# Optimization experiments

Hardware: AMD Instinct MI355X
Metric: run time of the kernel (lower is better)

## Reference

```python
import jax, jax.numpy as jnp
import numpy as np

H = 256
NUM_REL = 480
NUM_ENT = 23000
N_TRIPLES = 8192
T = 10  # cur_ts == path_len window


def _lin_params(key, din, dout):
    kw, _ = jax.random.split(key)
    W = jax.random.normal(kw, (din, dout), dtype=jnp.float32) * 0.02
    b = jnp.zeros((dout,), dtype=jnp.float32)
    return W, b


def setup_inputs() -> dict:
    key = jax.random.key(0)
    ks = jax.random.split(key, 16)
    pre_emb = jax.random.normal(ks[0], (NUM_ENT, H), dtype=jnp.float32)
    r_emb = jax.random.normal(ks[1], (NUM_REL, H), dtype=jnp.float32)
    # history counts: sparse non-negative (zeros are masked to -1e9 in softmax)
    part = jax.random.uniform(ks[2], (N_TRIPLES, T * NUM_REL), dtype=jnp.float32)
    mask = jax.random.uniform(ks[3], (N_TRIPLES, T * NUM_REL)) < 0.3
    partial_embeding = jnp.where(mask, part, 0.0)
    sub_idx = jax.random.randint(ks[4], (N_TRIPLES,), 0, NUM_ENT)
    rel_idx = jax.random.randint(ks[5], (N_TRIPLES,), 0, NUM_REL)
    obj_idx = jax.random.randint(ks[6], (N_TRIPLES,), 0, NUM_ENT)
    Wm1, bm1 = _lin_params(ks[7], H, 2 * H)
    Wm2, bm2 = _lin_params(ks[8], 2 * H, H)
    Wattn, battn = _lin_params(ks[9], H, H)
    Wh1, bh1 = _lin_params(ks[10], H, H)
    Wh2, bh2 = _lin_params(ks[11], H, H)
    Walign, balign = _lin_params(ks[12], H, H)
    Wih = jax.random.normal(ks[13], (H, 3 * H), dtype=jnp.float32) * 0.02
    Whh = jax.random.normal(ks[14], (H, 3 * H), dtype=jnp.float32) * 0.02
    bih = jnp.zeros((3 * H,), dtype=jnp.float32)
    bhh = jnp.zeros((3 * H,), dtype=jnp.float32)
    return dict(pre_emb=pre_emb, r_emb=r_emb, partial_embeding=partial_embeding,
                sub_idx=sub_idx, rel_idx=rel_idx, obj_idx=obj_idx, cur_ts=T,
                Wm1=Wm1, bm1=bm1, Wm2=Wm2, bm2=bm2, Wattn=Wattn, battn=battn,
                Wh1=Wh1, bh1=bh1, Wh2=Wh2, bh2=bh2, Walign=Walign, balign=balign,
                Wih=Wih, Whh=Whh, bih=bih, bhh=bhh)


def _gru_cell(x, h, Wih, Whh, bih, bhh):
    # torch.nn.GRUCell math
    gi = x @ Wih + bih
    gh = h @ Whh + bhh
    i_r, i_z, i_n = jnp.split(gi, 3, axis=-1)
    h_r, h_z, h_n = jnp.split(gh, 3, axis=-1)
    r = jax.nn.sigmoid(i_r + h_r)
    z = jax.nn.sigmoid(i_z + h_z)
    n = jnp.tanh(i_n + r * h_n)
    return (1.0 - z) * n + z * h


def reference(pre_emb, r_emb, partial_embeding, sub_idx, rel_idx, obj_idx, cur_ts,
              Wm1, bm1, Wm2, bm2, Wattn, battn, Wh1, bh1, Wh2, bh2,
              Walign, balign, Wih, Whh, bih, bhh):
    n = partial_embeding.shape[0]
    num_rel = r_emb.shape[0]
    t = cur_ts  # path window covers [0, cur_ts)
    # relation mapping
    mapped_rel = (r_emb @ Wm1 + bm1) @ Wm2 + bm2            # [R, H]
    q_rel = mapped_rel[rel_idx]                               # [N, H]
    # attention logits base (loop-invariant): q W_attn mapped_rel^T
    base = (q_rel @ Wattn + battn) @ mapped_rel.T            # [N, R]
    # [N, t*R] -> [t, N, R] time-major slices
    hist = partial_embeding[:, : t * num_rel].reshape(n, t, num_rel).swapaxes(0, 1)
    h0 = jnp.zeros((n, mapped_rel.shape[1]), dtype=pre_emb.dtype)

    def step(h, cur):
        attn = cur * base
        attn = jax.nn.softmax(jnp.where(attn == 0, -1e9, attn), axis=1)
        x = attn @ mapped_rel                                 # [N, H]
        return _gru_cell(x, h, Wih, Whh, bih, bhh), None

    gru_hidden, _ = jax.lax.scan(step, h0, hist)
    # predicted history + match loss
    predicted_hist = 0.1 * ((q_rel @ Wh1 + bh1) @ Wh2 + bh2) + q_rel
    match_loss = jnp.mean((predicted_hist - gru_hidden) ** 2)
    # forward_forth (distmult)
    h2 = _gru_cell(q_rel, predicted_hist, Wih, Whh, bih, bhh)  # [N, H]
    sub = pre_emb[sub_idx]
    score_ = ((sub @ Walign + balign) * h2) @ (pre_emb @ Walign + balign).T  # [N, E]
    # BCE(sigmoid(score_), one_hot(obj)): per-elem -y*logsig(s) - (1-y)*logsig(-s)
    pos = score_[jnp.arange(n), obj_idx]
    path_loss = (-jnp.sum(jax.nn.log_sigmoid(-score_)) - jnp.sum(pos)) / (score_.size)
    score = jax.nn.sigmoid(score_)
    return match_loss, path_loss, score
```

## Files before the change

### kernel.cpp

```cpp
#include <hip/hip_runtime.h>
#include <hip/hip_bf16.h>
#include <stdint.h>

#define DEV __device__ __forceinline__

typedef unsigned short u16;
typedef __attribute__((ext_vector_type(8))) short bf16x8;
typedef __attribute__((ext_vector_type(4))) float f32x4;
typedef __attribute__((ext_vector_type(4))) unsigned short u16x4;

constexpr int H  = 256;
constexpr int R  = 480;
constexpr int RP = 512;
constexpr int NE = 23000;
constexpr int NT = 8192;
constexpr int TT = 10;

DEV u16 f2b(float f) {
  union { float f; unsigned u; } x; x.f = f;
  unsigned u = x.u;
  return (u16)((u + 0x7fffu + ((u >> 16) & 1u)) >> 16);
}
DEV float b2f(u16 h) {
  union { unsigned u; float f; } x; x.u = ((unsigned)h) << 16;
  return x.f;
}

DEV void gload_lds16(const u16* g, u16* lds) {
  __builtin_amdgcn_global_load_lds(
      (const __attribute__((address_space(1))) unsigned int*)g,
      (__attribute__((address_space(3))) unsigned int*)lds, 16, 0, 0);
}

__launch_bounds__(256)
__global__ void stageA_k(const float* __restrict__ r_emb,
                         const float* __restrict__ Wm1, const float* __restrict__ bm1,
                         const float* __restrict__ Wm2, const float* __restrict__ bm2,
                         const float* __restrict__ Wattn, const float* __restrict__ battn,
                         const float* __restrict__ Wih,
                         const float* __restrict__ Wh1, const float* __restrict__ bh1,
                         const float* __restrict__ Wh2, const float* __restrict__ bh2,
                         const float* __restrict__ Whh, const float* __restrict__ bhh,
                         const float* __restrict__ bih, const float* __restrict__ Walign,
                         float* __restrict__ mapped, float* __restrict__ t1,
                         float* __restrict__ Pg, float* __restrict__ G2,
                         u16* __restrict__ MWT, u16* __restrict__ WhhT,
                         u16* __restrict__ WalignT, float* __restrict__ bsum) {
  __shared__ float re[256], hid[512], mp[256], p1l[256], Pl[256];
  const int j = threadIdx.x;
  if (blockIdx.x >= 480) {
    const int b = blockIdx.x - 480;
    if (b < 768) {
      WhhT[(size_t)b * 256 + j] = f2b(Whh[(size_t)j * 768 + b]);
    } else if (b < 1024) {
      const int n = b - 768;
      WalignT[(size_t)n * 256 + j] = f2b(Walign[(size_t)j * 256 + n]);
    } else {
      const int c = (b - 1024) * 256 + j;
      if (c < 768) bsum[c] = bih[c] + (c < 512 ? bhh[c] : 0.f);
    }
    return;
  }
  const int r = blockIdx.x;
  re[j] = r_emb[(size_t)r * 256 + j];
  __syncthreads();
  float s0 = bm1[j], s1 = bm1[j + 256];
  for (int k = 0; k < 256; ++k) {
    const float a = re[k];
    s0 += a * Wm1[(size_t)k * 512 + j];
    s1 += a * Wm1[(size_t)k * 512 + j + 256];
  }
  hid[j] = s0; hid[j + 256] = s1;
  __syncthreads();
  float m = bm2[j];
  for (int k = 0; k < 512; ++k) m += hid[k] * Wm2[(size_t)k * 256 + j];
  mp[j] = m; mapped[(size_t)r * 256 + j] = m;
  __syncthreads();
  float tv = battn[j];
  for (int k = 0; k < 256; ++k) tv += mp[k] * Wattn[(size_t)k * 256 + j];
  t1[(size_t)r * 256 + j] = tv;
  float mw0 = 0.f, mw1 = 0.f, mw2 = 0.f;
  for (int k = 0; k < 256; ++k) {
    const float a = mp[k];
    mw0 += a * Wih[(size_t)k * 768 + j];
    mw1 += a * Wih[(size_t)k * 768 + j + 256];
    mw2 += a * Wih[(size_t)k * 768 + j + 512];
  }
  MWT[(size_t)j * RP + r] = f2b(mw0);
  MWT[(size_t)(j + 256) * RP + r] = f2b(mw1);
  MWT[(size_t)(j + 512) * RP + r] = f2b(mw2);
  float pv = bh1[j];
  for (int k = 0; k < 256; ++k) pv += mp[k] * Wh1[(size_t)k * 256 + j];
  p1l[j] = pv;
  __syncthreads();
  float Pv = bh2[j];
  for (int k = 0; k < 256; ++k) Pv += p1l[k] * Wh2[(size_t)k * 256 + j];
  Pv = 0.1f * Pv + mp[j];
  Pl[j] = Pv; Pg[(size_t)r * 256 + j] = Pv;
  __syncthreads();
  float pw0 = bhh[j], pw1 = bhh[j + 256], pw2 = bhh[j + 512];
  for (int k = 0; k < 256; ++k) {
    const float a = Pl[k];
    pw0 += a * Whh[(size_t)k * 768 + j];
    pw1 += a * Whh[(size_t)k * 768 + j + 256];
    pw2 += a * Whh[(size_t)k * 768 + j + 512];
  }
  const float rg = 1.f / (1.f + __expf(-(mw0 + bih[j] + pw0)));
  const float zg = 1.f / (1.f + __expf(-(mw1 + bih[j + 256] + pw1)));
  const float ng = tanhf(mw2 + bih[j + 512] + rg * pw2);
  G2[(size_t)r * 256 + j] = (1.f - zg) * ng + zg * Pv;
}

__global__ void sgemm_bt_k(const float* __restrict__ A, const float* __restrict__ W,
                           float* __restrict__ C, int M, int N, int K) {
  const int idx = blockIdx.x * 256 + threadIdx.x;
  if (idx >= M * N) return;
  const int i = idx / N, j = idx % N;
  float s = 0.f;
  const float* a = A + (size_t)i * K;
  const float* w = W + (size_t)j * K;
  for (int k = 0; k < K; ++k) s += a[k] * w[k];
  C[idx] = s;
}

__global__ void softmax_all_k(const float* __restrict__ part, const float* __restrict__ B480,
                              const int* __restrict__ rel_idx, u16* __restrict__ attn) {
  const int task = blockIdx.x * 4 + (threadIdx.x >> 6);
  const int lane = threadIdx.x & 63;
  const int tt = task >> 13;
  const int i  = task & (NT - 1);
  const float* cur = part + (size_t)i * (TT * R) + (size_t)tt * R;
  const float* b = B480 + (size_t)rel_idx[i] * R;
  float v[8];
  float m = -3e38f;
  #pragma unroll
  for (int j = 0; j < 8; ++j) {
    const int r = lane + j * 64;
    float val = -1e9f;
    if (r < R) {
      const float c = cur[r];
      val = (c == 0.f) ? -1e9f : c * b[r];
      m = fmaxf(m, val);
    }
    v[j] = val;
  }
  #pragma unroll
  for (int o = 32; o; o >>= 1) m = fmaxf(m, __shfl_xor(m, o));
  float s = 0.f;
  #pragma unroll
  for (int j = 0; j < 8; ++j) {
    const int r = lane + j * 64;
    if (r < R) { v[j] = __expf(v[j] - m); s += v[j]; }
  }
  #pragma unroll
  for (int o = 32; o; o >>= 1) s += __shfl_xor(s, o);
  const float inv = 1.f / s;
  u16* arow = attn + (size_t)task * RP;
  #pragma unroll
  for (int j = 0; j < 8; ++j) {
    const int r = lane + j * 64;
    arow[r] = (r < R) ? f2b(v[j] * inv) : (u16)0;
  }
}

__launch_bounds__(256)
__global__ void scan_k(const u16* __restrict__ WhhT, const float* __restrict__ bhh,
                       const u16* __restrict__ gi_all, float* __restrict__ hbuf) {
  __shared__ __align__(16) u16 As[32 * 256];
  __shared__ __align__(16) u16 Bs[2][192 * 64];
  const int tid = threadIdx.x;
  const int lane = tid & 63;
  const int wv = tid >> 6;
  const int rf = wv >> 1;
  const int ch = wv & 1;
  const int fr = lane & 15;
  const int fq = lane >> 4;
  const int row_l = rf * 16 + fr;
  const int grow = blockIdx.x * 32 + row_l;
  const int sw = (fr & 7) * 8;

  auto stageB = [&](int buf, int cg, int k0) {
    #pragma unroll
    for (int it = 0; it < 6; ++it) {
      const int c = it * 256 + tid;
      const int vr = c >> 3, s = c & 7;
      const int vcol = ((vr >> 6) * 256) + cg * 64 + (vr & 63);
      gload_lds16(WhhT + (size_t)vcol * 256 + k0 + ((s ^ (vr & 7)) * 8),
                  &Bs[buf][(it * 256 + wv * 64) * 8]);
    }
  };

  float hreg[4][2][4];
  #pragma unroll
  for (int cg = 0; cg < 4; ++cg)
    #pragma unroll
    for (int nn = 0; nn < 2; ++nn)
      #pragma unroll
      for (int j = 0; j < 4; ++j) hreg[cg][nn][j] = 0.f;

  for (int t = 0; t < TT; ++t) {
    const u16* gi = gi_all + (size_t)t * NT * 768;
    #pragma unroll
    for (int cg = 0; cg < 4; ++cg) {
      f32x4 acc[6] = {};
      u16x4 gv[3][2];
      #pragma unroll
      for (int nn = 0; nn < 2; ++nn) {
        const int c = cg * 64 + ch * 32 + nn * 16 + fq * 4;
        const size_t gb = (size_t)grow * 768 + c;
        gv[0][nn] = *(const u16x4*)&gi[gb];
        gv[1][nn] = *(const u16x4*)&gi[gb + 256];
        gv[2][nn] = *(const u16x4*)&gi[gb + 512];
      }
      if (t > 0) {
        stageB(0, cg, 0);
        #pragma unroll
        for (int ki = 0; ki < 4; ++ki) {
          const int cb = ki & 1;
          if (ki < 3) {
            stageB(cb ^ 1, cg, (ki + 1) * 64);
            asm volatile("s_waitcnt vmcnt(6)" ::: "memory");
          } else {
            asm volatile("s_waitcnt vmcnt(0)" ::: "memory");
          }
          __builtin_amdgcn_sched_barrier(0);
          __builtin_amdgcn_s_barrier();
          #pragma unroll
          for (int kk = 0; kk < 2; ++kk) {
            const int ko = (ki * 64 + kk * 32 + fq * 8) ^ sw;
            const bf16x8 a = *(const bf16x8*)&As[row_l * 256 + ko];
            const int bo = (kk * 32 + fq * 8) ^ sw;
            #pragma unroll
            for (int g = 0; g < 3; ++g)
              #pragma unroll
              for (int nn = 0; nn < 2; ++nn) {
                const int vr = g * 64 + ch * 32 + nn * 16 + fr;
                const bf16x8 b = *(const bf16x8*)&Bs[cb][vr * 64 + bo];
                acc[g * 2 + nn] =
                    __builtin_amdgcn_mfma_f32_16x16x32_bf16(b, a, acc[g * 2 + nn], 0, 0, 0);
              }
          }
          __builtin_amdgcn_s_barrier();
        }
      }
      #pragma unroll
      for (int nn = 0; nn < 2; ++nn) {
        const int c = cg * 64 + ch * 32 + nn * 16 + fq * 4;
        const f32x4 bn = *(const f32x4*)&bhh[512 + c];
        #pragma unroll
        for (int j = 0; j < 4; ++j) {
          const float rg = 1.f / (1.f + __expf(-(b2f(gv[0][nn][j]) + acc[nn][j])));
          const float zg = 1.f / (1.f + __expf(-(b2f(gv[1][nn][j]) + acc[2 + nn][j])));
          const float ng = tanhf(b2f(gv[2][nn][j]) + rg * (acc[4 + nn][j] + bn[j]));
          hreg[cg][nn][j] = (1.f - zg) * ng + zg * hreg[cg][nn][j];
        }
      }
    }
    #pragma unroll
    for (int cg = 0; cg < 4; ++cg)
      #pragma unroll
      for (int nn = 0; nn < 2; ++nn) {
        const int c = cg * 64 + ch * 32 + nn * 16 + fq * 4;
        u16x4 o;
        #pragma unroll
        for (int j = 0; j < 4; ++j) o[j] = f2b(hreg[cg][nn][j]);
        *(u16x4*)&As[row_l * 256 + (c ^ sw)] = o;
        if (t == TT - 1) {
          f32x4 hv;
          #pragma unroll
          for (int j = 0; j < 4; ++j) hv[j] = hreg[cg][nn][j];
          *(f32x4*)&hbuf[(size_t)grow * 256 + c] = hv;
        }
      }
    __syncthreads();
  }
}

__global__ void gather_sub_k(const float* __restrict__ pre, const int* __restrict__ sub,
                             u16* __restrict__ sb) {
  const int q = blockIdx.x * 256 + threadIdx.x;
  const int i = q >> 6, c = (q & 63) * 4;
  const f32x4 v = *(const f32x4*)&pre[(size_t)sub[i] * H + c];
  u16x4 o;
  #pragma unroll
  for (int j = 0; j < 4; ++j) o[j] = f2b(v[j]);
  *(u16x4*)&sb[(size_t)q * 4] = o;
}
__global__ void cvt_pre_k(const float* __restrict__ pre, u16* __restrict__ pb) {
  const int q = blockIdx.x * 256 + threadIdx.x;
  const f32x4 v = *(const f32x4*)&pre[(size_t)q * 4];
  u16x4 o;
  #pragma unroll
  for (int j = 0; j < 4; ++j) o[j] = f2b(v[j]);
  *(u16x4*)&pb[(size_t)q * 4] = o;
}

__global__ void pos_k(const u16* __restrict__ lhs, const u16* __restrict__ alT,
                      const int* __restrict__ obj, float* __restrict__ pos) {
  const int row = blockIdx.x * 4 + (threadIdx.x >> 6);
  const int lane = threadIdx.x & 63;
  const u16x4 av = *(const u16x4*)&lhs[(size_t)row * H + lane * 4];
  const u16x4 bv = *(const u16x4*)&alT[(size_t)obj[row] * H + lane * 4];
  float s = 0.f;
  #pragma unroll
  for (int j = 0; j < 4; ++j) s += b2f(av[j]) * b2f(bv[j]);
  #pragma unroll
  for (int o = 32; o; o >>= 1) s += __shfl_down(s, o);
  if (lane == 0) pos[row] = s;
}

__global__ void finalize_k(const float* __restrict__ mp, const float* __restrict__ sp,
                           const float* __restrict__ pos, float* __restrict__ out) {
  const int tid = threadIdx.x;
  float s1 = 0.f, s2 = 0.f, s3 = 0.f;
  for (int i = tid; i < 128; i += 256) s1 += mp[i];
  for (int i = tid; i < 11520; i += 256) s2 += sp[i];
  for (int i = tid; i < 8192; i += 256) s3 += pos[i];
  #pragma unroll
  for (int o = 32; o; o >>= 1) {
    s1 += __shfl_down(s1, o); s2 += __shfl_down(s2, o); s3 += __shfl_down(s3, o);
  }
  __shared__ float r1[4], r2[4], r3[4];
  if ((tid & 63) == 0) { r1[tid >> 6] = s1; r2[tid >> 6] = s2; r3[tid >> 6] = s3; }
  __syncthreads();
  if (tid == 0) {
    const float a = r1[0] + r1[1] + r1[2] + r1[3];
    const float b = r2[0] + r2[1] + r2[2] + r2[3];
    const float c = r3[0] + r3[1] + r3[2] + r3[3];
    out[0] = a / 2097152.f;
    out[1] = (b - c) / 188416000.f;
  }
}

template <int MODE>
__launch_bounds__(256)
__global__ void gemm_k(const u16* __restrict__ A, const u16* __restrict__ Bt,
                       const float* __restrict__ bias,
                       float* __restrict__ Cf, u16* __restrict__ Cb,
                       int M, int N, int K,
                       float* __restrict__ out2, float* __restrict__ part,
                       const int* __restrict__ rel_idx, const float* __restrict__ Pf,
                       const float* __restrict__ G2f, const float* __restrict__ hf) {
  __shared__ __align__(16) u16 As[2][128 * 64];
  __shared__ __align__(16) u16 Bs[2][128 * 64];
  __shared__ float red[4];
  const int tid = threadIdx.x;
  const int lane = tid & 63;
  const int wv = tid >> 6;
  const int nbx = gridDim.x;
  int flat = blockIdx.y * nbx + blockIdx.x;
  const int nwg = nbx * gridDim.y;
  if ((nwg & 7) == 0) flat = (flat & 7) * (nwg >> 3) + (flat >> 3);
  const int bx = flat % nbx;
  const int by = flat / nbx;
  const int m0 = by * 128;
  const int n0 = bx * 128;
  const int wm = (wv >> 1) * 64;
  const int wn = (wv & 1) * 64;
  const int fr = lane & 15;
  const int fq = lane >> 4;
  const int sw = (lane & 7) * 8;
  f32x4 acc[4][4] = {};

  auto stage = [&](int buf, int k0) {
    #pragma unroll
    for (int it = 0; it < 4; ++it) {
      const int c = it * 256 + tid;
      const int row = c >> 3, s = c & 7;
      const int sc = (s ^ (row & 7)) * 8;
      int gr = m0 + row; gr = gr < M ? gr : M - 1;
      gload_lds16(A + (size_t)gr * K + k0 + sc, &As[buf][(it * 256 + wv * 64) * 8]);
      int nr = n0 + row; nr = nr < N ? nr : N - 1;
      gload_lds16(Bt + (size_t)nr * K + k0 + sc, &Bs[buf][(it * 256 + wv * 64) * 8]);
    }
  };

  stage(0, 0);
  const int nsteps = K >> 6;
  for (int kt = 0; kt < nsteps; ++kt) {
    const int cb = kt & 1;
    if (kt + 1 < nsteps) {
      stage(cb ^ 1, (kt + 1) * 64);
      asm volatile("s_waitcnt vmcnt(8)" ::: "memory");
    } else {
      asm volatile("s_waitcnt vmcnt(0)" ::: "memory");
    }
    __builtin_amdgcn_sched_barrier(0);
    __builtin_amdgcn_s_barrier();
    #pragma unroll
    for (int kk = 0; kk < 2; ++kk) {
      const int ko = (kk * 32 + fq * 8) ^ sw;
      bf16x8 a[4], b[4];
      #pragma unroll
      for (int mi = 0; mi < 4; ++mi)
        a[mi] = *(const bf16x8*)&As[cb][(wm + mi * 16 + fr) * 64 + ko];
      #pragma unroll
      for (int ni = 0; ni < 4; ++ni)
        b[ni] = *(const bf16x8*)&Bs[cb][(wn + ni * 16 + fr) * 64 + ko];
      #pragma unroll
      for (int mi = 0; mi < 4; ++mi)
        #pragma unroll
        for (int ni = 0; ni < 4; ++ni)
          acc[mi][ni] = __builtin_amdgcn_mfma_f32_16x16x32_bf16(b[ni], a[mi], acc[mi][ni], 0, 0, 0);
    }
    __builtin_amdgcn_s_barrier();
  }

  float local = 0.f;
  #pragma unroll
  for (int mi = 0; mi < 4; ++mi) {
    const int rowm = m0 + wm + mi * 16 + fr;
    int rel = 0;
    if (MODE == 2) rel = rel_idx[rowm];
    #pragma unroll
    for (int ni = 0; ni < 4; ++ni) {
      const int col = n0 + wn + ni * 16 + fq * 4;
      if (rowm < M && col < N) {
        f32x4 v = acc[mi][ni];
        if (MODE == 0) {
          if (bias != nullptr) {
            const f32x4 bv = *(const f32x4*)&bias[col];
            #pragma unroll
            for (int j = 0; j < 4; ++j) v[j] += bv[j];
          }
          if (Cf) *(f32x4*)&Cf[(size_t)rowm * N + col] = v;
          if (Cb) {
            u16x4 o;
            #pragma unroll
            for (int j = 0; j < 4; ++j) o[j] = f2b(v[j]);
            *(u16x4*)&Cb[(size_t)rowm * N + col] = o;
          }
        } else if (MODE == 1) {
          f32x4 sg;
          #pragma unroll
          for (int j = 0; j < 4; ++j) {
            const float s = v[j];
            const float sig = 1.f / (1.f + __expf(-s));
            sg[j] = sig;
            const float om = 1.f - sig;
            local += (om > 0.f) ? -__logf(om) : s;
          }
          *(f32x4*)&out2[(size_t)rowm * N + col] = sg;
        } else {
          const f32x4 bv = *(const f32x4*)&bias[col];
          const f32x4 Pv = *(const f32x4*)&Pf[(size_t)rel * H + col];
          const f32x4 Gv = *(const f32x4*)&G2f[(size_t)rel * H + col];
          const f32x4 hv = *(const f32x4*)&hf[(size_t)rowm * H + col];
          u16x4 o;
          #pragma unroll
          for (int j = 0; j < 4; ++j) {
            const float d = Pv[j] - hv[j];
            local += d * d;
            o[j] = f2b((v[j] + bv[j]) * Gv[j]);
          }
          *(u16x4*)&Cb[(size_t)rowm * N + col] = o;
        }
      }
    }
  }
  if (MODE != 0) {
    #pragma unroll
    for (int o = 32; o; o >>= 1) local += __shfl_down(local, o);
    if (lane == 0) red[wv] = local;
    __syncthreads();
    if (tid == 0) part[blockIdx.y * gridDim.x + blockIdx.x] = red[0] + red[1] + red[2] + red[3];
  }
}

extern "C" void kernel_launch(void* const* d_in, const int* in_sizes, int n_in,
                              void* d_out, int out_size, void* d_ws, size_t ws_size,
                              hipStream_t stream) {
  const float* pre_emb = (const float*)d_in[0];
  const float* r_emb   = (const float*)d_in[1];
  const float* part_e  = (const float*)d_in[2];
  const int*   sub_idx = (const int*)d_in[3];
  const int*   rel_idx = (const int*)d_in[4];
  const int*   obj_idx = (const int*)d_in[5];
  const float* Wm1 = (const float*)d_in[7];  const float* bm1 = (const float*)d_in[8];
  const float* Wm2 = (const float*)d_in[9];  const float* bm2 = (const float*)d_in[10];
  const float* Wattn = (const float*)d_in[11]; const float* battn = (const float*)d_in[12];
  const float* Wh1 = (const float*)d_in[13]; const float* bh1 = (const float*)d_in[14];
  const float* Wh2 = (const float*)d_in[15]; const float* bh2 = (const float*)d_in[16];
  const float* Walign = (const float*)d_in[17]; const float* balign = (const float*)d_in[18];
  const float* Wih = (const float*)d_in[19]; const float* Whh = (const float*)d_in[20];
  const float* bih = (const float*)d_in[21]; const float* bhh = (const float*)d_in[22];
  float* out = (float*)d_out;

  char* w = (char*)d_ws;
  size_t off = 0;
  auto alloc = [&](size_t bytes) -> void* {
    off = (off + 255) & ~(size_t)255;
    void* p = w + off;
    off += bytes;
    return p;
  };
  float* mapped = (float*)alloc((size_t)R * H * 4);
  float* t1     = (float*)alloc((size_t)R * H * 4);
  float* B480   = (float*)alloc((size_t)R * R * 4);
  float* P      = (float*)alloc((size_t)R * H * 4);
  float* G2     = (float*)alloc((size_t)R * H * 4);
  u16* MWT      = (u16*)alloc((size_t)768 * RP * 2);
  u16* WhhT     = (u16*)alloc((size_t)768 * H * 2);
  u16* WalignT  = (u16*)alloc((size_t)H * H * 2);
  float* bsum   = (float*)alloc(768 * 4);
  float* hbuf   = (float*)alloc((size_t)NT * H * 4);
  u16* lhs_b    = (u16*)alloc((size_t)NT * H * 2);
  u16* sub_b    = (u16*)alloc((size_t)NT * H * 2);
  u16* pre_b    = (u16*)alloc((size_t)NE * H * 2);
  u16* alT      = (u16*)alloc((size_t)NE * H * 2);
  float* mpart  = (float*)alloc(128 * 4);
  float* spart  = (float*)alloc(11520 * 4);
  float* posar  = (float*)alloc(8192 * 4);
  u16* attn_all = (u16*)alloc((size_t)TT * NT * RP * 2);
  u16* gi_all   = (u16*)alloc((size_t)TT * NT * 768 * 2);
  if (off > ws_size) return;

  hipMemsetAsync(MWT, 0, (size_t)768 * RP * 2, stream);
  stageA_k<<<480 + 1027, 256, 0, stream>>>(
      r_emb, Wm1, bm1, Wm2, bm2, Wattn, battn, Wih, Wh1, bh1, Wh2, bh2,
      Whh, bhh, bih, Walign, mapped, t1, P, G2, MWT, WhhT, WalignT, bsum);
  sgemm_bt_k<<<(R * R + 255) / 256, 256, 0, stream>>>(t1, mapped, B480, R, R, H);

  softmax_all_k<<<TT * (NT / 4), 256, 0, stream>>>(part_e, B480, rel_idx, attn_all);
  gemm_k<0><<<dim3(6, TT * (NT / 128)), 256, 0, stream>>>(
      attn_all, MWT, bsum, nullptr, gi_all, TT * NT, 768, RP,
      nullptr, nullptr, nullptr, nullptr, nullptr, nullptr);
  scan_k<<<NT / 32, 256, 0, stream>>>(WhhT, bhh, gi_all, hbuf);

  gather_sub_k<<<NT / 4, 256, 0, stream>>>(pre_emb, sub_idx, sub_b);
  gemm_k<2><<<dim3(2, 64), 256, 0, stream>>>(
      sub_b, WalignT, balign, nullptr, lhs_b, NT, H, H,
      nullptr, mpart, rel_idx, P, G2, hbuf);

  cvt_pre_k<<<NE / 4, 256, 0, stream>>>(pre_emb, pre_b);
  gemm_k<0><<<dim3(2, 180), 256, 0, stream>>>(
      pre_b, WalignT, balign, nullptr, alT, NE, H, H,
      nullptr, nullptr, nullptr, nullptr, nullptr, nullptr);

  gemm_k<1><<<dim3(180, 64), 256, 0, stream>>>(
      lhs_b, alT, nullptr, nullptr, nullptr, NT, NE, H,
      out + 2, spart, nullptr, nullptr, nullptr, nullptr);

  pos_k<<<2048, 256, 0, stream>>>(lhs_b, alT, obj_idx, posar);
  finalize_k<<<1, 256, 0, stream>>>(mpart, spart, posar, out);
}
```

Baseline: 1.094 ms.

## Vectorize stage-A matvecs, softmax and sgemm; fold pos score into score GEMM

Several independent changes land together. The stage-A per-relation matvecs are rewritten to use float4 loads with split-K LDS reductions, and the MWT padding zeroing moves into extra blocks of that kernel in place of a full hipMemset. The softmax and the small sgemm now use float4 loads and stores. The separate pos_k kernel is removed, and the positive-score subtraction is folded into the MODE 1 GEMM epilogue through a per-row obj index compare. Together these aim to cut launch count and memory-access inefficiency in the small stages, at the cost of an extra compare in the hot score epilogue.

```diff
diff --git a/kernel.cpp b/kernel.cpp
--- a/kernel.cpp
+++ b/kernel.cpp
@@ -46,7 +46,6 @@
                          float* __restrict__ Pg, float* __restrict__ G2,
                          u16* __restrict__ MWT, u16* __restrict__ WhhT,
                          u16* __restrict__ WalignT, float* __restrict__ bsum) {
-  __shared__ float re[256], hid[512], mp[256], p1l[256], Pl[256];
   const int j = threadIdx.x;
   if (blockIdx.x >= 480) {
     const int b = blockIdx.x - 480;
@@ -55,60 +54,111 @@
     } else if (b < 1024) {
       const int n = b - 768;
       WalignT[(size_t)n * 256 + j] = f2b(Walign[(size_t)j * 256 + n]);
-    } else {
+    } else if (b < 1027) {
       const int c = (b - 1024) * 256 + j;
       if (c < 768) bsum[c] = bih[c] + (c < 512 ? bhh[c] : 0.f);
+    } else {
+      const int row = (b - 1027) * 256 + j;
+      if (row < 768) {
+        const u16x4 z = {0, 0, 0, 0};
+        #pragma unroll
+        for (int c = 480; c < 512; c += 4) *(u16x4*)&MWT[(size_t)row * RP + c] = z;
+      }
     }
     return;
   }
+  __shared__ float re[256], hid[512], mp[256], p1l[256], Pl[256];
+  __shared__ float mwl[768], pwl[768];
+  __shared__ f32x4 red4[256];
   const int r = blockIdx.x;
+  const f32x4 z4 = {0.f, 0.f, 0.f, 0.f};
   re[j] = r_emb[(size_t)r * 256 + j];
   __syncthreads();
-  float s0 = bm1[j], s1 = bm1[j + 256];
-  for (int k = 0; k < 256; ++k) {
-    const float a = re[k];
-    s0 += a * Wm1[(size_t)k * 512 + j];
-    s1 += a * Wm1[(size_t)k * 512 + j + 256];
-  }
-  hid[j] = s0; hid[j + 256] = s1;
+  {
+    const int q = j & 127, g = j >> 7;
+    f32x4 acc = (g == 0) ? *(const f32x4*)&bm1[q * 4] : z4;
+    for (int k = g * 128; k < g * 128 + 128; ++k)
+      acc += re[k] * *(const f32x4*)&Wm1[(size_t)k * 512 + q * 4];
+    red4[j] = acc;
+    __syncthreads();
+    if (j < 128) *(f32x4*)&hid[j * 4] = red4[j] + red4[j + 128];
+    __syncthreads();
+  }
+  {
+    const int q = j & 63, g = j >> 6;
+    f32x4 acc = (g == 0) ? *(const f32x4*)&bm2[q * 4] : z4;
+    for (int k = g * 128; k < g * 128 + 128; ++k)
+      acc += hid[k] * *(const f32x4*)&Wm2[(size_t)k * 256 + q * 4];
+    red4[j] = acc;
+    __syncthreads();
+    if (j < 64) {
+      const f32x4 s = red4[j] + red4[j + 64] + red4[j + 128] + red4[j + 192];
+      *(f32x4*)&mp[j * 4] = s;
+      *(f32x4*)&mapped[(size_t)r * 256 + j * 4] = s;
+    }
+    __syncthreads();
+  }
+  {
+    const int q = j & 63, g = j >> 6;
+    f32x4 acc = (g == 0) ? *(const f32x4*)&battn[q * 4] : z4;
+    for (int k = g * 64; k < g * 64 + 64; ++k)
+      acc += mp[k] * *(const f32x4*)&Wattn[(size_t)k * 256 + q * 4];
+    red4[j] = acc;
+    __syncthreads();
+    if (j < 64)
+      *(f32x4*)&t1[(size_t)r * 256 + j * 4] =
+          red4[j] + red4[j + 64] + red4[j + 128] + red4[j + 192];
+    __syncthreads();
+  }
+  if (j < 192) {
+    f32x4 acc = z4;
+    for (int k = 0; k < 256; ++k)
+      acc += mp[k] * *(const f32x4*)&Wih[(size_t)k * 768 + j * 4];
+    *(f32x4*)&mwl[j * 4] = acc;
+    #pragma unroll
+    for (int c = 0; c < 4; ++c) MWT[(size_t)(j * 4 + c) * RP + r] = f2b(acc[c]);
+  }
   __syncthreads();
-  float m = bm2[j];
-  for (int k = 0; k < 512; ++k) m += hid[k] * Wm2[(size_t)k * 256 + j];
-  mp[j] = m; mapped[(size_t)r * 256 + j] = m;
+  {
+    const int q = j & 63, g = j >> 6;
+    f32x4 acc = (g == 0) ? *(const f32x4*)&bh1[q * 4] : z4;
+    for (int k = g * 64; k < g * 64 + 64; ++k)
+      acc += mp[k] * *(const f32x4*)&Wh1[(size_t)k * 256 + q * 4];
+    red4[j] = acc;
+    __syncthreads();
+    if (j < 64) *(f32x4*)&p1l[j * 4] = red4[j] + red4[j + 64] + red4[j + 128] + red4[j + 192];
+    __syncthreads();
+  }
+  {
+    const int q = j & 63, g = j >> 6;
+    f32x4 acc = (g == 0) ? *(const f32x4*)&bh2[q * 4] : z4;
+    for (int k = g * 64; k < g * 64 + 64; ++k)
+      acc += p1l[k] * *(const f32x4*)&Wh2[(size_t)k * 256 + q * 4];
+    red4[j] = acc;
+    __syncthreads();
+    if (j < 64) {
+      f32x4 s = red4[j] + red4[j + 64] + red4[j + 128] + red4[j + 192];
+      const f32x4 mv = *(const f32x4*)&mp[j * 4];
+      #pragma unroll
+      for (int c = 0; c < 4; ++c) s[c] = 0.1f * s[c] + mv[c];
+      *(f32x4*)&Pl[j * 4] = s;
+      *(f32x4*)&Pg[(size_t)r * 256 + j * 4] = s;
+    }
+    __syncthreads();
+  }
+  if (j < 192) {
+    f32x4 acc = *(const f32x4*)&bhh[j * 4];
+    for (int k = 0; k < 256; ++k)
+      acc += Pl[k] * *(const f32x4*)&Whh[(size_t)k * 768 + j * 4];
+    *(f32x4*)&pwl[j * 4] = acc;
+  }
   __syncthreads();
-  float tv = battn[j];
-  for (int k = 0; k < 256; ++k) tv += mp[k] * Wattn[(size_t)k * 256 + j];
-  t1[(size_t)r * 256 + j] = tv;
-  float mw0 = 0.f, mw1 = 0.f, mw2 = 0.f;
-  for (int k = 0; k < 256; ++k) {
-    const float a = mp[k];
-    mw0 += a * Wih[(size_t)k * 768 + j];
-    mw1 += a * Wih[(size_t)k * 768 + j + 256];
-    mw2 += a * Wih[(size_t)k * 768 + j + 512];
-  }
-  MWT[(size_t)j * RP + r] = f2b(mw0);
-  MWT[(size_t)(j + 256) * RP + r] = f2b(mw1);
-  MWT[(size_t)(j + 512) * RP + r] = f2b(mw2);
-  float pv = bh1[j];
-  for (int k = 0; k < 256; ++k) pv += mp[k] * Wh1[(size_t)k * 256 + j];
-  p1l[j] = pv;
-  __syncthreads();
-  float Pv = bh2[j];
-  for (int k = 0; k < 256; ++k) Pv += p1l[k] * Wh2[(size_t)k * 256 + j];
-  Pv = 0.1f * Pv + mp[j];
-  Pl[j] = Pv; Pg[(size_t)r * 256 + j] = Pv;
-  __syncthreads();
-  float pw0 = bhh[j], pw1 = bhh[j + 256], pw2 = bhh[j + 512];
-  for (int k = 0; k < 256; ++k) {
-    const float a = Pl[k];
-    pw0 += a * Whh[(size_t)k * 768 + j];
-    pw1 += a * Whh[(size_t)k * 768 + j + 256];
-    pw2 += a * Whh[(size_t)k * 768 + j + 512];
-  }
-  const float rg = 1.f / (1.f + __expf(-(mw0 + bih[j] + pw0)));
-  const float zg = 1.f / (1.f + __expf(-(mw1 + bih[j + 256] + pw1)));
-  const float ng = tanhf(mw2 + bih[j + 512] + rg * pw2);
-  G2[(size_t)r * 256 + j] = (1.f - zg) * ng + zg * Pv;
+  {
+    const float rg = 1.f / (1.f + __expf(-(mwl[j] + bih[j] + pwl[j])));
+    const float zg = 1.f / (1.f + __expf(-(mwl[j + 256] + bih[j + 256] + pwl[j + 256])));
+    const float ng = tanhf(mwl[j + 512] + bih[j + 512] + rg * pwl[j + 512]);
+    G2[(size_t)r * 256 + j] = (1.f - zg) * ng + zg * Pl[j];
+  }
 }
 
 __global__ void sgemm_bt_k(const float* __restrict__ A, const float* __restrict__ W,
@@ -116,11 +166,11 @@
   const int idx = blockIdx.x * 256 + threadIdx.x;
   if (idx >= M * N) return;
   const int i = idx / N, j = idx % N;
-  float s = 0.f;
-  const float* a = A + (size_t)i * K;
-  const float* w = W + (size_t)j * K;
-  for (int k = 0; k < K; ++k) s += a[k] * w[k];
-  C[idx] = s;
+  const f32x4* a4 = (const f32x4*)(A + (size_t)i * K);
+  const f32x4* w4 = (const f32x4*)(W + (size_t)j * K);
+  f32x4 acc = {0.f, 0.f, 0.f, 0.f};
+  for (int k = 0; k < K / 4; ++k) acc += a4[k] * w4[k];
+  C[idx] = acc[0] + acc[1] + acc[2] + acc[3];
 }
 
 __global__ void softmax_all_k(const float* __restrict__ part, const float* __restrict__ B480,
@@ -131,35 +181,47 @@
   const int i  = task & (NT - 1);
   const float* cur = part + (size_t)i * (TT * R) + (size_t)tt * R;
   const float* b = B480 + (size_t)rel_idx[i] * R;
-  float v[8];
+  f32x4 v[2];
   float m = -3e38f;
-  #pragma unroll
-  for (int j = 0; j < 8; ++j) {
-    const int r = lane + j * 64;
-    float val = -1e9f;
-    if (r < R) {
-      const float c = cur[r];
-      val = (c == 0.f) ? -1e9f : c * b[r];
-      m = fmaxf(m, val);
-    }
-    v[j] = val;
+  const bool act1 = lane < 56;
+  #pragma unroll
+  for (int jj = 0; jj < 2; ++jj) {
+    const int r0 = jj * 256 + lane * 4;
+    f32x4 val = {-1e9f, -1e9f, -1e9f, -1e9f};
+    if (jj == 0 || act1) {
+      const f32x4 c4 = *(const f32x4*)&cur[r0];
+      const f32x4 b4 = *(const f32x4*)&b[r0];
+      #pragma unroll
+      for (int x = 0; x < 4; ++x) {
+        val[x] = (c4[x] == 0.f) ? -1e9f : c4[x] * b4[x];
+        m = fmaxf(m, val[x]);
+      }
+    }
+    v[jj] = val;
   }
   #pragma unroll
   for (int o = 32; o; o >>= 1) m = fmaxf(m, __shfl_xor(m, o));
   float s = 0.f;
   #pragma unroll
-  for (int j = 0; j < 8; ++j) {
-    const int r = lane + j * 64;
-    if (r < R) { v[j] = __expf(v[j] - m); s += v[j]; }
+  for (int jj = 0; jj < 2; ++jj) {
+    if (jj == 0 || act1) {
+      #pragma unroll
+      for (int x = 0; x < 4; ++x) { v[jj][x] = __expf(v[jj][x] - m); s += v[jj][x]; }
+    }
   }
   #pragma unroll
   for (int o = 32; o; o >>= 1) s += __shfl_xor(s, o);
   const float inv = 1.f / s;
   u16* arow = attn + (size_t)task * RP;
   #pragma unroll
-  for (int j = 0; j < 8; ++j) {
-    const int r = lane + j * 64;
-    arow[r] = (r < R) ? f2b(v[j] * inv) : (u16)0;
+  for (int jj = 0; jj < 2; ++jj) {
+    const int r0 = jj * 256 + lane * 4;
+    u16x4 o = {0, 0, 0, 0};
+    if (jj == 0 || act1) {
+      #pragma unroll
+      for (int x = 0; x < 4; ++x) o[x] = f2b(v[jj][x] * inv);
+    }
+    *(u16x4*)&arow[r0] = o;
   }
 }
 
@@ -295,40 +357,24 @@
   *(u16x4*)&pb[(size_t)q * 4] = o;
 }
 
-__global__ void pos_k(const u16* __restrict__ lhs, const u16* __restrict__ alT,
-                      const int* __restrict__ obj, float* __restrict__ pos) {
-  const int row = blockIdx.x * 4 + (threadIdx.x >> 6);
-  const int lane = threadIdx.x & 63;
-  const u16x4 av = *(const u16x4*)&lhs[(size_t)row * H + lane * 4];
-  const u16x4 bv = *(const u16x4*)&alT[(size_t)obj[row] * H + lane * 4];
-  float s = 0.f;
-  #pragma unroll
-  for (int j = 0; j < 4; ++j) s += b2f(av[j]) * b2f(bv[j]);
-  #pragma unroll
-  for (int o = 32; o; o >>= 1) s += __shfl_down(s, o);
-  if (lane == 0) pos[row] = s;
-}
-
 __global__ void finalize_k(const float* __restrict__ mp, const float* __restrict__ sp,
-                           const float* __restrict__ pos, float* __restrict__ out) {
+                           float* __restrict__ out) {
   const int tid = threadIdx.x;
-  float s1 = 0.f, s2 = 0.f, s3 = 0.f;
+  float s1 = 0.f, s2 = 0.f;
   for (int i = tid; i < 128; i += 256) s1 += mp[i];
   for (int i = tid; i < 11520; i += 256) s2 += sp[i];
-  for (int i = tid; i < 8192; i += 256) s3 += pos[i];
   #pragma unroll
   for (int o = 32; o; o >>= 1) {
-    s1 += __shfl_down(s1, o); s2 += __shfl_down(s2, o); s3 += __shfl_down(s3, o);
-  }
-  __shared__ float r1[4], r2[4], r3[4];
-  if ((tid & 63) == 0) { r1[tid >> 6] = s1; r2[tid >> 6] = s2; r3[tid >> 6] = s3; }
+    s1 += __shfl_down(s1, o); s2 += __shfl_down(s2, o);
+  }
+  __shared__ float r1[4], r2[4];
+  if ((tid & 63) == 0) { r1[tid >> 6] = s1; r2[tid >> 6] = s2; }
   __syncthreads();
   if (tid == 0) {
     const float a = r1[0] + r1[1] + r1[2] + r1[3];
     const float b = r2[0] + r2[1] + r2[2] + r2[3];
-    const float c = r3[0] + r3[1] + r3[2] + r3[3];
     out[0] = a / 2097152.f;
-    out[1] = (b - c) / 188416000.f;
+    out[1] = b / 188416000.f;
   }
 }
 
@@ -339,7 +385,7 @@
                        float* __restrict__ Cf, u16* __restrict__ Cb,
                        int M, int N, int K,
                        float* __restrict__ out2, float* __restrict__ part,
-                       const int* __restrict__ rel_idx, const float* __restrict__ Pf,
+                       const int* __restrict__ idxv, const float* __restrict__ Pf,
                        const float* __restrict__ G2f, const float* __restrict__ hf) {
   __shared__ __align__(16) u16 As[2][128 * 64];
   __shared__ __align__(16) u16 Bs[2][128 * 64];
@@ -410,8 +456,8 @@
   #pragma unroll
   for (int mi = 0; mi < 4; ++mi) {
     const int rowm = m0 + wm + mi * 16 + fr;
-    int rel = 0;
-    if (MODE == 2) rel = rel_idx[rowm];
+    int iv = 0;
+    if (MODE != 0) iv = idxv[rowm < M ? rowm : M - 1];
     #pragma unroll
     for (int ni = 0; ni < 4; ++ni) {
       const int col = n0 + wn + ni * 16 + fq * 4;
@@ -439,12 +485,13 @@
             sg[j] = sig;
             const float om = 1.f - sig;
             local += (om > 0.f) ? -__logf(om) : s;
+            if (col + j == iv) local -= s;
           }
           *(f32x4*)&out2[(size_t)rowm * N + col] = sg;
         } else {
           const f32x4 bv = *(const f32x4*)&bias[col];
-          const f32x4 Pv = *(const f32x4*)&Pf[(size_t)rel * H + col];
-          const f32x4 Gv = *(const f32x4*)&G2f[(size_t)rel * H + col];
+          const f32x4 Pv = *(const f32x4*)&Pf[(size_t)iv * H + col];
+          const f32x4 Gv = *(const f32x4*)&G2f[(size_t)iv * H + col];
           const f32x4 hv = *(const f32x4*)&hf[(size_t)rowm * H + col];
           u16x4 o;
           #pragma unroll
@@ -510,13 +557,11 @@
   u16* alT      = (u16*)alloc((size_t)NE * H * 2);
   float* mpart  = (float*)alloc(128 * 4);
   float* spart  = (float*)alloc(11520 * 4);
-  float* posar  = (float*)alloc(8192 * 4);
   u16* attn_all = (u16*)alloc((size_t)TT * NT * RP * 2);
   u16* gi_all   = (u16*)alloc((size_t)TT * NT * 768 * 2);
   if (off > ws_size) return;
 
-  hipMemsetAsync(MWT, 0, (size_t)768 * RP * 2, stream);
-  stageA_k<<<480 + 1027, 256, 0, stream>>>(
+  stageA_k<<<480 + 1030, 256, 0, stream>>>(
       r_emb, Wm1, bm1, Wm2, bm2, Wattn, battn, Wih, Wh1, bh1, Wh2, bh2,
       Whh, bhh, bih, Walign, mapped, t1, P, G2, MWT, WhhT, WalignT, bsum);
   sgemm_bt_k<<<(R * R + 255) / 256, 256, 0, stream>>>(t1, mapped, B480, R, R, H);
@@ -539,8 +584,7 @@
 
   gemm_k<1><<<dim3(180, 64), 256, 0, stream>>>(
       lhs_b, alT, nullptr, nullptr, nullptr, NT, NE, H,
-      out + 2, spart, nullptr, nullptr, nullptr, nullptr);
-
-  pos_k<<<2048, 256, 0, stream>>>(lhs_b, alT, obj_idx, posar);
-  finalize_k<<<1, 256, 0, stream>>>(mpart, spart, posar, out);
-}
+      out + 2, spart, obj_idx, nullptr, nullptr, nullptr);
+
+  finalize_k<<<1, 256, 0, stream>>>(mpart, spart, out);
+}
```

Result: no change. 1.090 ms (-0.3%).
